# Kernel optimization log

Hardware: AMD Instinct MI355X
Metric: run time of the kernel (lower is better)

The kernel has to match this reference:

```python
import jax, jax.numpy as jnp
import numpy as np

VOCAB = 32000
PENTA_DIM = 512
DIM = 512
NUM_HEADS = 8
HEAD_DIM = DIM // NUM_HEADS
CANTOR_DEPTH = 8
K_NEIGHBORS = 64  # local_window, adaptive_window=False
BATCH = 2
SEQ = 2048
EPS = 1e-6


def cantor_coords_from_pentachora(pentachora):
    """Vectorized GeometricCantorFingerprinter over [V,5,D] -> [V] coords in [0,1]."""
    V = pentachora.shape[0]
    # pairwise squared distances between the 5 vertices: [V,5,5]
    diff = pentachora[:, :, None, :] - pentachora[:, None, :, :]
    dist_sq = jnp.sum(diff * diff, axis=-1)
    # Cayley-Menger matrix [V,6,6]
    M = jnp.zeros((V, 6, 6), dtype=pentachora.dtype)
    M = M.at[:, 0, 1:].set(1.0)
    M = M.at[:, 1:, 0].set(1.0)
    M = M.at[:, 1:, 1:].set(dist_sq)
    det = jnp.linalg.det(M)
    volume = jnp.sqrt(jnp.clip(-det / 9216.0, 0.0))
    # edge statistics: 10 upper-triangular edges
    iu, ju = np.triu_indices(5, 1)
    edge_len = jnp.sqrt(dist_sq[:, iu, ju])  # [V,10]
    mean_edge = edge_len.mean(axis=-1)
    std_edge = edge_len.std(axis=-1, ddof=1)  # torch.std is unbiased
    # vertex spread: std (ddof=1) of distances to centroid
    centroid = pentachora.mean(axis=1, keepdims=True)
    cd = jnp.linalg.norm(pentachora - centroid, axis=-1)  # [V,5]
    spread = cd.std(axis=-1, ddof=1)
    volume_norm = jax.nn.sigmoid(volume * 10.0)
    edge_ratio = jax.nn.sigmoid(std_edge / (mean_edge + 1e-6))
    spread_norm = jax.nn.sigmoid(spread)
    x = jnp.clip(volume_norm * 0.4 + edge_ratio * 0.3 + spread_norm * 0.3, EPS, 1.0 - EPS)
    bump = (volume_norm + edge_ratio + spread_norm) * 0.01
    cantor_val = jnp.zeros_like(x)
    factor = 0.5
    for _ in range(CANTOR_DEPTH):  # small fixed unroll
        x_scaled = x * 3.0
        digit = jnp.floor(x_scaled)  # x in (0,1) so trunc==floor
        x_frac = x_scaled - digit
        cantor_val = cantor_val + (digit == 2.0).astype(x.dtype) * factor
        x = jnp.clip(x_frac + bump, EPS, 1.0 - EPS)
        factor *= 0.5
    return jnp.clip(cantor_val, 0.0, 1.0)


def setup_inputs() -> dict:
    key = jax.random.key(0)
    ks = jax.random.split(key, 8)
    pentachora = jax.random.normal(ks[0], (VOCAB, 5, PENTA_DIM), dtype=jnp.float32)
    x = jax.random.normal(ks[1], (BATCH, SEQ, DIM), dtype=jnp.float32)
    token_ids = jax.random.randint(ks[2], (SEQ,), 0, VOCAB)
    s = 1.0 / np.sqrt(DIM)
    Wqkv = jax.random.normal(ks[3], (DIM, 3 * DIM), dtype=jnp.float32) * s
    bqkv = jnp.zeros((3 * DIM,), dtype=jnp.float32)
    Wout = jax.random.normal(ks[4], (DIM, DIM), dtype=jnp.float32) * s
    bout = jnp.zeros((DIM,), dtype=jnp.float32)
    return {"pentachora": pentachora, "x": x, "token_ids": token_ids,
            "Wqkv": Wqkv, "bqkv": bqkv, "Wout": Wout, "bout": bout}


def reference(pentachora, x, token_ids, Wqkv, bqkv, Wout, bout):
    coords = cantor_coords_from_pentachora(pentachora)  # [V]
    c = coords[token_ids]  # [S] per-token Cantor coordinates
    # routing: k nearest tokens in 1D Cantor space (smallest |ci - cj|)
    dist = jnp.abs(c[:, None] - c[None, :])  # [S,S]
    _, routes = jax.lax.top_k(-dist, K_NEIGHBORS)  # [S,K]
    B, S, D = x.shape
    qkv = x @ Wqkv + bqkv  # [B,S,3D]
    qkv = qkv.reshape(B, S, 3, NUM_HEADS, HEAD_DIM).transpose(2, 0, 3, 1, 4)
    q, k, v = qkv[0], qkv[1], qkv[2]  # [B,H,S,hd]
    k_g = k[:, :, routes, :]  # [B,H,S,K,hd]
    v_g = v[:, :, routes, :]
    scale = 1.0 / np.sqrt(HEAD_DIM)
    scores = jnp.einsum('bhqd,bhqkd->bhqk', q, k_g) * scale
    attn = jax.nn.softmax(scores, axis=-1)
    out = jnp.einsum('bhqk,bhqkd->bhqd', attn, v_g)  # [B,H,S,hd]
    out = out.transpose(0, 2, 1, 3).reshape(B, S, D)
    return out @ Wout + bout
```

## Files before the change

kernel.cpp:

```cpp
#include <hip/hip_runtime.h>
#include <math.h>


typedef unsigned short u16;
typedef short short8 __attribute__((ext_vector_type(8)));
typedef u16 u16x8 __attribute__((ext_vector_type(8)));
typedef float floatx4 __attribute__((ext_vector_type(4)));

#define NVOCAB 32000
#define NSEQ 2048

__device__ inline float b2f(u16 u){
  union{unsigned int i; float f;} x; x.i = ((unsigned int)u)<<16; return x.f;
}
__device__ inline u16 f2b(float f){
  union{float f; unsigned int u;} x; x.f = f;
  unsigned int u = x.u;
  u += 0x7fffu + ((u >> 16) & 1u);
  return (u16)(u >> 16);
}
__device__ inline double shfl_xor_d(double v, int m){
  union{double d; int i[2];} x; x.d = v;
  x.i[0] = __shfl_xor(x.i[0], m, 64);
  x.i[1] = __shfl_xor(x.i[1], m, 64);
  return x.d;
}
__device__ inline int detect_flag(const u16* __restrict__ p){
  int lane = threadIdx.x & 63;
  u16 u = p[lane*2];
  int e = (u >> 7) & 0xff;
  unsigned long long m = __ballot(e >= 96 && e <= 144);
  return (m == ~0ull) ? 1 : 0;
}

__global__ __launch_bounds__(256) void prep_kernel(const void* __restrict__ x,
                                                   const void* __restrict__ W1,
                                                   const void* __restrict__ W2,
                                                   const u16* __restrict__ penta,
                                                   u16* __restrict__ xb,
                                                   u16* __restrict__ Wt1,
                                                   u16* __restrict__ Wt2){
  int f = detect_flag(penta);
  int bid = blockIdx.x;
  if (bid < 1024){
    size_t i = ((size_t)bid*256 + threadIdx.x)*8;
    if (f){
      *(u16x8*)(xb+i) = *(const u16x8*)((const u16*)x + i);
    } else {
      const float* xf = (const float*)x + i;
      float4 a = *(const float4*)xf;
      float4 b = *(const float4*)(xf+4);
      u16x8 o;
      o[0]=f2b(a.x); o[1]=f2b(a.y); o[2]=f2b(a.z); o[3]=f2b(a.w);
      o[4]=f2b(b.x); o[5]=f2b(b.y); o[6]=f2b(b.z); o[7]=f2b(b.w);
      *(u16x8*)(xb+i) = o;
    }
    return;
  }
  int idx = bid - 1024;
  int bx = idx & 63;
  int k0 = (idx >> 6) * 32;
  __shared__ u16 tile[32][33];
  const int K = 512;
  const void* W; u16* Wt; int N, n0;
  if (bx < 48){ W = W1; Wt = Wt1; N = 1536; n0 = bx*32; }
  else        { W = W2; Wt = Wt2; N = 512;  n0 = (bx-48)*32; }
  int tx = threadIdx.x & 31, ty = threadIdx.x >> 5;
  #pragma unroll
  for (int i=0;i<32;i+=8){
    int k = k0+ty+i, n = n0+tx;
    u16 v = f ? ((const u16*)W)[(size_t)k*N + n]
              : f2b(((const float*)W)[(size_t)k*N + n]);
    tile[ty+i][tx] = v;
  }
  __syncthreads();
  #pragma unroll
  for (int i=0;i<32;i+=8){
    Wt[(size_t)(n0+ty+i)*K + k0+tx] = tile[tx][ty+i];
  }
}

__global__ __launch_bounds__(256) void penta_coords_kernel(const void* __restrict__ penta,
                                                           const int* __restrict__ tok,
                                                           int* __restrict__ ctok){
  int f = detect_flag((const u16*)penta);
  int slot = blockIdx.x*4 + (threadIdx.x>>6);
  int w = tok[slot];
  int lane = threadIdx.x & 63;
  float pf[5][8];
  if (f){
    const u16* base = (const u16*)penta + (size_t)w*2560 + lane*8;
    #pragma unroll
    for (int i=0;i<5;i++){
      u16x8 u = *(const u16x8*)(base + i*512);
      #pragma unroll
      for (int j=0;j<8;j++) pf[i][j] = b2f(u[j]);
    }
  } else {
    const float* base = (const float*)penta + (size_t)w*2560 + lane*8;
    #pragma unroll
    for (int i=0;i<5;i++){
      float4 f0 = *(const float4*)(base + i*512);
      float4 f1 = *(const float4*)(base + i*512 + 4);
      pf[i][0]=f0.x; pf[i][1]=f0.y; pf[i][2]=f0.z; pf[i][3]=f0.w;
      pf[i][4]=f1.x; pf[i][5]=f1.y; pf[i][6]=f1.z; pf[i][7]=f1.w;
    }
  }
  double acc[15];
  #pragma unroll
  for (int k=0;k<15;k++) acc[k]=0.0;
  #pragma unroll
  for (int j=0;j<8;j++){
    double p[5];
    #pragma unroll
    for (int i=0;i<5;i++) p[i] = (double)pf[i][j];
    double mean = (p[0]+p[1]+p[2]+p[3]+p[4])*0.2;
    int idx=0;
    #pragma unroll
    for (int a=0;a<5;a++)
      #pragma unroll
      for (int b=a+1;b<5;b++){ double d=p[a]-p[b]; acc[idx++] += d*d; }
    #pragma unroll
    for (int i=0;i<5;i++){ double d=p[i]-mean; acc[10+i] += d*d; }
  }
  #pragma unroll
  for (int k=0;k<15;k++){
    double s = acc[k];
    for (int off=32; off; off>>=1) s += shfl_xor_d(s, off);
    acc[k]=s;
  }
  if (lane != 0) return;
  double ds[10], cd2[5];
  #pragma unroll
  for (int k=0;k<10;k++) ds[k]=acc[k];
  #pragma unroll
  for (int k=0;k<5;k++) cd2[k]=acc[10+k];
  double M[6][6];
  M[0][0]=1.0; M[0][1]=0.0; M[0][2]=ds[0]; M[0][3]=ds[1]; M[0][4]=ds[2]; M[0][5]=ds[3];
  M[1][0]=0.0; M[1][1]=1.0; M[1][2]=1.0;   M[1][3]=1.0;   M[1][4]=1.0;   M[1][5]=1.0;
  M[2][0]=1.0; M[2][1]=ds[0]; M[2][2]=0.0;   M[2][3]=ds[4]; M[2][4]=ds[5]; M[2][5]=ds[6];
  M[3][0]=1.0; M[3][1]=ds[1]; M[3][2]=ds[4]; M[3][3]=0.0;   M[3][4]=ds[7]; M[3][5]=ds[8];
  M[4][0]=1.0; M[4][1]=ds[2]; M[4][2]=ds[5]; M[4][3]=ds[7]; M[4][4]=0.0;   M[4][5]=ds[9];
  M[5][0]=1.0; M[5][1]=ds[3]; M[5][2]=ds[6]; M[5][3]=ds[8]; M[5][4]=ds[9]; M[5][5]=0.0;
  double det=1.0;
  #pragma unroll
  for (int c=0;c<6;c++){
    double pv = M[c][c];
    det *= pv;
    double inv = 1.0/pv;
    #pragma unroll
    for (int r=c+1;r<6;r++){
      double fq = M[r][c]*inv;
      #pragma unroll
      for (int cc=c+1;cc<6;cc++) M[r][cc] -= fq*M[c][cc];
    }
  }
  double volume = sqrt(fmax(det/9216.0, 0.0));
  double vn = 1.0/(1.0+exp(-10.0*volume));
  double me=0.0, e[10];
  #pragma unroll
  for (int k=0;k<10;k++){ e[k]=sqrt(ds[k]); me+=e[k]; }
  me *= 0.1;
  double var=0.0;
  #pragma unroll
  for (int k=0;k<10;k++){ double d=e[k]-me; var+=d*d; }
  double se = sqrt(var/9.0);
  double er = 1.0/(1.0+exp(-(se/(me+1e-6))));
  double mc=0.0, cd[5];
  #pragma unroll
  for (int k=0;k<5;k++){ cd[k]=sqrt(cd2[k]); mc+=cd[k]; }
  mc *= 0.2;
  double v2=0.0;
  #pragma unroll
  for (int k=0;k<5;k++){ double d=cd[k]-mc; v2+=d*d; }
  double sp = sqrt(v2/4.0);
  double sn = 1.0/(1.0+exp(-sp));
  const double EPSd = 1e-6;
  double x = 0.4*vn + 0.3*er + 0.3*sn;
  x = fmin(fmax(x, EPSd), 1.0-EPSd);
  double bump = (vn+er+sn)*0.01;
  double cv=0.0, factor=0.5;
  #pragma unroll
  for (int it=0; it<8; it++){
    double xs = x*3.0;
    double frac = xs - floor(xs);
    if (xs >= 2.0) cv += factor;
    x = fmin(fmax(frac + bump, EPSd), 1.0-EPSd);
    factor *= 0.5;
  }
  cv = fmin(fmax(cv,0.0),1.0);
  ctok[slot] = (int)(cv*256.0 + 0.5);
}

__global__ __launch_bounds__(256) void routes_kernel(const int* __restrict__ ctok,
                                                     int* __restrict__ repq,
                                                     int* __restrict__ routes){
  __shared__ int cs[NSEQ];
  __shared__ int hist[256];
  __shared__ int scn[256];
  __shared__ int cnts[256];
  __shared__ int params[3];
  __shared__ int repsh;
  int tid = threadIdx.x;
  int q = blockIdx.x;
  for (int j=tid; j<NSEQ; j+=256) cs[j] = ctok[j];
  hist[tid] = 0;
  if (tid==0){ params[2]=0; repsh=0x7fffffff; }
  __syncthreads();
  int cq = cs[q];
  int base = tid*8;
  {
    int myrep = 0x7fffffff;
    #pragma unroll
    for (int i=0;i<8;i++){
      if (cs[base+i]==cq && myrep==0x7fffffff) myrep = base+i;
    }
    if (myrep != 0x7fffffff) atomicMin(&repsh, myrep);
  }
  __syncthreads();
  if (tid==0) repq[q] = repsh;
  if (repsh != q) return;
  int dloc[8];
  #pragma unroll
  for (int i=0;i<8;i++){
    int d = cs[base+i] - cq; d = d<0 ? -d : d;
    dloc[i] = d;
    atomicAdd(&hist[d], 1);
  }
  __syncthreads();
  scn[tid] = hist[tid];
  __syncthreads();
  #pragma unroll
  for (int off=1; off<256; off<<=1){
    int cur = scn[tid];
    int add = (tid>=off) ? scn[tid-off] : 0;
    __syncthreads();
    scn[tid] = cur + add;
    __syncthreads();
  }
  {
    int incl = scn[tid];
    int prev = (tid==0) ? 0 : scn[tid-1];
    if (incl >= 64 && prev < 64){ params[0]=tid; params[1]=64-prev; }
  }
  __syncthreads();
  int T=params[0], need=params[1];
  int ceq=0;
  #pragma unroll
  for (int i=0;i<8;i++) ceq += (dloc[i]==T) ? 1 : 0;
  cnts[tid]=ceq;
  __syncthreads();
  #pragma unroll
  for (int off=1; off<256; off<<=1){
    int cur = cnts[tid];
    int add = (tid>=off) ? cnts[tid-off] : 0;
    __syncthreads();
    cnts[tid] = cur + add;
    __syncthreads();
  }
  int rank = cnts[tid] - ceq;
  int* rq = routes + q*64;
  #pragma unroll
  for (int i=0;i<8;i++){
    int d = dloc[i];
    bool sel = false;
    if (d < T) sel = true;
    else if (d == T){ sel = (rank < need); rank++; }
    if (sel){
      int pos = atomicAdd(&params[2], 1);
      rq[pos] = base + i;
    }
  }
}

template<int C_FOLLOW>
__global__ __launch_bounds__(256) void gemm_direct(const u16* __restrict__ A,
    const u16* __restrict__ Wt, const void* __restrict__ bias, void* __restrict__ Cout,
    const u16* __restrict__ penta, int M, int N, int K)
{
  int f = detect_flag(penta);
  bool c_bf16 = C_FOLLOW ? (f==1) : true;
  int tid = threadIdx.x;
  int wv = tid>>6, lane = tid&63, lr = lane&15, lq = lane>>4;
  int m0 = blockIdx.y<<6, n0 = blockIdx.x<<6;
  const u16* Arow = A  + (size_t)(m0 + (wv<<4) + lr)*K + (lq<<3);
  const u16* Wr0  = Wt + (size_t)(n0 + lr)*K + (lq<<3);
  size_t wstep = (size_t)16*K;
  floatx4 acc[4];
  #pragma unroll
  for (int t=0;t<4;t++) acc[t] = (floatx4){0.f,0.f,0.f,0.f};
  #pragma unroll 4
  for (int k0=0;k0<K;k0+=32){
    short8 af = *(const short8*)(Arow + k0);
    #pragma unroll
    for (int t4=0;t4<4;t4++){
      short8 bfv = *(const short8*)(Wr0 + (size_t)t4*wstep + k0);
      acc[t4] = __builtin_amdgcn_mfma_f32_16x16x32_bf16(af, bfv, acc[t4], 0, 0, 0);
    }
  }
  #pragma unroll
  for (int t4=0;t4<4;t4++){
    #pragma unroll
    for (int r=0;r<4;r++){
      int m = m0 + (wv<<4) + (lq<<2) + r;
      int n = n0 + (t4<<4) + lr;
      float bv = f ? b2f(((const u16*)bias)[n]) : ((const float*)bias)[n];
      float val = acc[t4][r] + bv;
      if (c_bf16) ((u16*)Cout)[(size_t)m*N + n] = f2b(val);
      else        ((float*)Cout)[(size_t)m*N + n] = val;
    }
  }
}

__global__ __launch_bounds__(256) void attn_kernel(const u16* __restrict__ qkv,
                                                   const int* __restrict__ routes,
                                                   const int* __restrict__ repq,
                                                   u16* __restrict__ outa){
  __shared__ float sc[4][8*65];
  __shared__ int rbuf[4][64];
  int tid = threadIdx.x;
  int wv = tid>>6, lane = tid&63;
  int bq = blockIdx.x*4 + wv;
  int b = bq >> 11;
  int q = bq & 2047;
  rbuf[wv][lane] = routes[(repq[q]<<6) + lane];
  int h8 = lane>>3;
  const u16* kb = qkv + (size_t)(b<<11)*1536;
  float qv[8];
  {
    u16x8 qraw = *(const u16x8*)(kb + (size_t)q*1536 + lane*8);
    #pragma unroll
    for (int t=0;t<8;t++) qv[t] = b2f(qraw[t]);
  }
  __syncthreads();
  for (int j=0;j<64;j++){
    int rj = rbuf[wv][j];
    u16x8 kraw = *(const u16x8*)(kb + (size_t)rj*1536 + 512 + lane*8);
    float p = 0.f;
    #pragma unroll
    for (int t=0;t<8;t++) p = fmaf(b2f(kraw[t]), qv[t], p);
    p += __shfl_xor(p, 1, 64);
    p += __shfl_xor(p, 2, 64);
    p += __shfl_xor(p, 4, 64);
    if ((lane&7)==0) sc[wv][h8*65 + j] = p * 0.125f;
  }
  __syncthreads();
  {
    int jg = (lane&7)<<3;
    float sv[8];
    float m = -1e30f;
    #pragma unroll
    for (int t=0;t<8;t++){ sv[t] = sc[wv][h8*65 + jg + t]; m = fmaxf(m, sv[t]); }
    m = fmaxf(m, __shfl_xor(m, 1, 64));
    m = fmaxf(m, __shfl_xor(m, 2, 64));
    m = fmaxf(m, __shfl_xor(m, 4, 64));
    float s = 0.f;
    #pragma unroll
    for (int t=0;t<8;t++){ sv[t] = expf(sv[t]-m); s += sv[t]; }
    s += __shfl_xor(s, 1, 64);
    s += __shfl_xor(s, 2, 64);
    s += __shfl_xor(s, 4, 64);
    float inv = 1.f/s;
    #pragma unroll
    for (int t=0;t<8;t++) sc[wv][h8*65 + jg + t] = sv[t]*inv;
  }
  __syncthreads();
  int dg = (lane&7)<<3;
  const u16* vb = kb + 1024 + (h8<<6) + dg;
  float acc8[8];
  #pragma unroll
  for (int t=0;t<8;t++) acc8[t]=0.f;
  for (int j=0;j<64;j++){
    float p = sc[wv][h8*65 + j];
    u16x8 v8 = *(const u16x8*)(vb + (size_t)rbuf[wv][j]*1536);
    #pragma unroll
    for (int t=0;t<8;t++) acc8[t] = fmaf(p, b2f(v8[t]), acc8[t]);
  }
  u16x8 o;
  #pragma unroll
  for (int t=0;t<8;t++) o[t] = f2b(acc8[t]);
  *(u16x8*)(outa + (size_t)bq*512 + (h8<<6) + dg) = o;
}

extern "C" void kernel_launch(void* const* d_in, const int* in_sizes, int n_in,
                              void* d_out, int out_size, void* d_ws, size_t ws_size,
                              hipStream_t stream) {
  const void* penta = d_in[0];
  const void* x     = d_in[1];
  const int*  tok   = (const int*)d_in[2];
  const void* Wqkv  = d_in[3];
  const void* bqkv  = d_in[4];
  const void* Wout  = d_in[5];
  const void* bout  = d_in[6];

  char* ws = (char*)d_ws;
  int*    ctok   = (int*)   (ws + 0);
  int*    repq   = (int*)   (ws + 8192);
  int*    routes = (int*)   (ws + 16384);
  u16*    xb     = (u16*)   (ws + 1048576);
  u16*    Wt1    = (u16*)   (ws + 5242880);
  u16*    Wt2    = (u16*)   (ws + 6815744);
  u16*    qkv    = (u16*)   (ws + 7340032);
  u16*    attn   = (u16*)   (ws + 19922944);

  prep_kernel<<<dim3(2048), dim3(256), 0, stream>>>(x, Wqkv, Wout, (const u16*)penta, xb, Wt1, Wt2);
  penta_coords_kernel<<<dim3(512), dim3(256), 0, stream>>>(penta, tok, ctok);
  routes_kernel<<<dim3(2048), dim3(256), 0, stream>>>(ctok, repq, routes);
  gemm_direct<0><<<dim3(24,64), dim3(256), 0, stream>>>(xb, Wt1, bqkv, (void*)qkv, (const u16*)penta, 4096, 1536, 512);
  attn_kernel<<<dim3(1024), dim3(256), 0, stream>>>(qkv, routes, repq, attn);
  gemm_direct<1><<<dim3(8,64), dim3(256), 0, stream>>>(attn, Wt2, bout, d_out, (const u16*)penta, 4096, 512, 512);
}
```

Before: 518.0 us.

## Fuse prep and coords kernels, skip bf16 x copy, double GEMM M-tile

Merges the input conversion/transpose kernel with the per-token pentachoron coordinate kernel into one launch, removing a kernel boundary. When inputs are already bf16 the x copy is skipped and the QKV GEMM reads x directly. The GEMM now computes a 128-row tile per block (two 16-row MFMA strips per wave), so each B fragment load is reused twice, at the cost of more accumulator registers and half as many blocks.

Result: faster. 489.9 us (-5.4%).

```diff
diff --git a/kernel.cpp b/kernel.cpp
--- a/kernel.cpp
+++ b/kernel.cpp
@@ -33,58 +33,54 @@
   return (m == ~0ull) ? 1 : 0;
 }
 
-__global__ __launch_bounds__(256) void prep_kernel(const void* __restrict__ x,
-                                                   const void* __restrict__ W1,
-                                                   const void* __restrict__ W2,
-                                                   const u16* __restrict__ penta,
-                                                   u16* __restrict__ xb,
-                                                   u16* __restrict__ Wt1,
-                                                   u16* __restrict__ Wt2){
-  int f = detect_flag(penta);
+__global__ __launch_bounds__(256) void prep_coords_kernel(const void* __restrict__ x,
+                                                          const void* __restrict__ W1,
+                                                          const void* __restrict__ W2,
+                                                          const void* __restrict__ penta,
+                                                          const int* __restrict__ tok,
+                                                          u16* __restrict__ xb,
+                                                          u16* __restrict__ Wt1,
+                                                          u16* __restrict__ Wt2,
+                                                          int* __restrict__ ctok){
+  __shared__ u16 tile[32][33];
+  int f = detect_flag((const u16*)penta);
   int bid = blockIdx.x;
   if (bid < 1024){
+    if (f) return;
     size_t i = ((size_t)bid*256 + threadIdx.x)*8;
-    if (f){
-      *(u16x8*)(xb+i) = *(const u16x8*)((const u16*)x + i);
-    } else {
-      const float* xf = (const float*)x + i;
-      float4 a = *(const float4*)xf;
-      float4 b = *(const float4*)(xf+4);
-      u16x8 o;
-      o[0]=f2b(a.x); o[1]=f2b(a.y); o[2]=f2b(a.z); o[3]=f2b(a.w);
-      o[4]=f2b(b.x); o[5]=f2b(b.y); o[6]=f2b(b.z); o[7]=f2b(b.w);
-      *(u16x8*)(xb+i) = o;
-    }
+    const float* xf = (const float*)x + i;
+    float4 a = *(const float4*)xf;
+    float4 b = *(const float4*)(xf+4);
+    u16x8 o;
+    o[0]=f2b(a.x); o[1]=f2b(a.y); o[2]=f2b(a.z); o[3]=f2b(a.w);
+    o[4]=f2b(b.x); o[5]=f2b(b.y); o[6]=f2b(b.z); o[7]=f2b(b.w);
+    *(u16x8*)(xb+i) = o;
     return;
   }
-  int idx = bid - 1024;
-  int bx = idx & 63;
-  int k0 = (idx >> 6) * 32;
-  __shared__ u16 tile[32][33];
-  const int K = 512;
-  const void* W; u16* Wt; int N, n0;
-  if (bx < 48){ W = W1; Wt = Wt1; N = 1536; n0 = bx*32; }
-  else        { W = W2; Wt = Wt2; N = 512;  n0 = (bx-48)*32; }
-  int tx = threadIdx.x & 31, ty = threadIdx.x >> 5;
-  #pragma unroll
-  for (int i=0;i<32;i+=8){
-    int k = k0+ty+i, n = n0+tx;
-    u16 v = f ? ((const u16*)W)[(size_t)k*N + n]
-              : f2b(((const float*)W)[(size_t)k*N + n]);
-    tile[ty+i][tx] = v;
-  }
-  __syncthreads();
-  #pragma unroll
-  for (int i=0;i<32;i+=8){
-    Wt[(size_t)(n0+ty+i)*K + k0+tx] = tile[tx][ty+i];
-  }
-}
-
-__global__ __launch_bounds__(256) void penta_coords_kernel(const void* __restrict__ penta,
-                                                           const int* __restrict__ tok,
-                                                           int* __restrict__ ctok){
-  int f = detect_flag((const u16*)penta);
-  int slot = blockIdx.x*4 + (threadIdx.x>>6);
+  if (bid < 2048){
+    int idx = bid - 1024;
+    int bx = idx & 63;
+    int k0 = (idx >> 6) * 32;
+    const int K = 512;
+    const void* W; u16* Wt; int N, n0;
+    if (bx < 48){ W = W1; Wt = Wt1; N = 1536; n0 = bx*32; }
+    else        { W = W2; Wt = Wt2; N = 512;  n0 = (bx-48)*32; }
+    int tx = threadIdx.x & 31, ty = threadIdx.x >> 5;
+    #pragma unroll
+    for (int i=0;i<32;i+=8){
+      int k = k0+ty+i, n = n0+tx;
+      u16 v = f ? ((const u16*)W)[(size_t)k*N + n]
+                : f2b(((const float*)W)[(size_t)k*N + n]);
+      tile[ty+i][tx] = v;
+    }
+    __syncthreads();
+    #pragma unroll
+    for (int i=0;i<32;i+=8){
+      Wt[(size_t)(n0+ty+i)*K + k0+tx] = tile[tx][ty+i];
+    }
+    return;
+  }
+  int slot = (bid-2048)*4 + (threadIdx.x>>6);
   int w = tok[slot];
   int lane = threadIdx.x & 63;
   float pf[5][8];
@@ -176,16 +172,16 @@
   double sp = sqrt(v2/4.0);
   double sn = 1.0/(1.0+exp(-sp));
   const double EPSd = 1e-6;
-  double x = 0.4*vn + 0.3*er + 0.3*sn;
-  x = fmin(fmax(x, EPSd), 1.0-EPSd);
+  double xx = 0.4*vn + 0.3*er + 0.3*sn;
+  xx = fmin(fmax(xx, EPSd), 1.0-EPSd);
   double bump = (vn+er+sn)*0.01;
   double cv=0.0, factor=0.5;
   #pragma unroll
   for (int it=0; it<8; it++){
-    double xs = x*3.0;
+    double xs = xx*3.0;
     double frac = xs - floor(xs);
     if (xs >= 2.0) cv += factor;
-    x = fmin(fmax(frac + bump, EPSd), 1.0-EPSd);
+    xx = fmin(fmax(frac + bump, EPSd), 1.0-EPSd);
     factor *= 0.5;
   }
   cv = fmin(fmax(cv,0.0),1.0);
@@ -274,40 +270,50 @@
 }
 
 template<int C_FOLLOW>
-__global__ __launch_bounds__(256) void gemm_direct(const u16* __restrict__ A,
-    const u16* __restrict__ Wt, const void* __restrict__ bias, void* __restrict__ Cout,
+__global__ __launch_bounds__(256) void gemm_direct(const u16* __restrict__ Af1,
+    const u16* __restrict__ Af0, const u16* __restrict__ Wt,
+    const void* __restrict__ bias, void* __restrict__ Cout,
     const u16* __restrict__ penta, int M, int N, int K)
 {
   int f = detect_flag(penta);
+  const u16* A = f ? Af1 : Af0;
   bool c_bf16 = C_FOLLOW ? (f==1) : true;
   int tid = threadIdx.x;
   int wv = tid>>6, lane = tid&63, lr = lane&15, lq = lane>>4;
-  int m0 = blockIdx.y<<6, n0 = blockIdx.x<<6;
-  const u16* Arow = A  + (size_t)(m0 + (wv<<4) + lr)*K + (lq<<3);
-  const u16* Wr0  = Wt + (size_t)(n0 + lr)*K + (lq<<3);
+  int m0 = blockIdx.y<<7, n0 = blockIdx.x<<6;
+  const u16* Arow0 = A  + (size_t)(m0 + (wv<<5) + lr)*K + (lq<<3);
+  const u16* Arow1 = Arow0 + (size_t)16*K;
+  const u16* Wr0   = Wt + (size_t)(n0 + lr)*K + (lq<<3);
   size_t wstep = (size_t)16*K;
-  floatx4 acc[4];
-  #pragma unroll
-  for (int t=0;t<4;t++) acc[t] = (floatx4){0.f,0.f,0.f,0.f};
+  floatx4 acc[2][4];
+  #pragma unroll
+  for (int mt=0;mt<2;mt++)
+    #pragma unroll
+    for (int t=0;t<4;t++) acc[mt][t] = (floatx4){0.f,0.f,0.f,0.f};
   #pragma unroll 4
   for (int k0=0;k0<K;k0+=32){
-    short8 af = *(const short8*)(Arow + k0);
+    short8 af0 = *(const short8*)(Arow0 + k0);
+    short8 af1 = *(const short8*)(Arow1 + k0);
     #pragma unroll
     for (int t4=0;t4<4;t4++){
       short8 bfv = *(const short8*)(Wr0 + (size_t)t4*wstep + k0);
-      acc[t4] = __builtin_amdgcn_mfma_f32_16x16x32_bf16(af, bfv, acc[t4], 0, 0, 0);
-    }
-  }
-  #pragma unroll
-  for (int t4=0;t4<4;t4++){
-    #pragma unroll
-    for (int r=0;r<4;r++){
-      int m = m0 + (wv<<4) + (lq<<2) + r;
-      int n = n0 + (t4<<4) + lr;
-      float bv = f ? b2f(((const u16*)bias)[n]) : ((const float*)bias)[n];
-      float val = acc[t4][r] + bv;
-      if (c_bf16) ((u16*)Cout)[(size_t)m*N + n] = f2b(val);
-      else        ((float*)Cout)[(size_t)m*N + n] = val;
+      acc[0][t4] = __builtin_amdgcn_mfma_f32_16x16x32_bf16(af0, bfv, acc[0][t4], 0, 0, 0);
+      acc[1][t4] = __builtin_amdgcn_mfma_f32_16x16x32_bf16(af1, bfv, acc[1][t4], 0, 0, 0);
+    }
+  }
+  #pragma unroll
+  for (int mt=0;mt<2;mt++){
+    #pragma unroll
+    for (int t4=0;t4<4;t4++){
+      #pragma unroll
+      for (int r=0;r<4;r++){
+        int m = m0 + (wv<<5) + (mt<<4) + (lq<<2) + r;
+        int n = n0 + (t4<<4) + lr;
+        float bv = f ? b2f(((const u16*)bias)[n]) : ((const float*)bias)[n];
+        float val = acc[mt][t4][r] + bv;
+        if (c_bf16) ((u16*)Cout)[(size_t)m*N + n] = f2b(val);
+        else        ((float*)Cout)[(size_t)m*N + n] = val;
+      }
     }
   }
 }
@@ -403,10 +409,9 @@
   u16*    qkv    = (u16*)   (ws + 7340032);
   u16*    attn   = (u16*)   (ws + 19922944);
 
-  prep_kernel<<<dim3(2048), dim3(256), 0, stream>>>(x, Wqkv, Wout, (const u16*)penta, xb, Wt1, Wt2);
-  penta_coords_kernel<<<dim3(512), dim3(256), 0, stream>>>(penta, tok, ctok);
+  prep_coords_kernel<<<dim3(2560), dim3(256), 0, stream>>>(x, Wqkv, Wout, penta, tok, xb, Wt1, Wt2, ctok);
   routes_kernel<<<dim3(2048), dim3(256), 0, stream>>>(ctok, repq, routes);
-  gemm_direct<0><<<dim3(24,64), dim3(256), 0, stream>>>(xb, Wt1, bqkv, (void*)qkv, (const u16*)penta, 4096, 1536, 512);
+  gemm_direct<0><<<dim3(24,32), dim3(256), 0, stream>>>((const u16*)x, xb, Wt1, bqkv, (void*)qkv, (const u16*)penta, 4096, 1536, 512);
   attn_kernel<<<dim3(1024), dim3(256), 0, stream>>>(qkv, routes, repq, attn);
-  gemm_direct<1><<<dim3(8,64), dim3(256), 0, stream>>>(attn, Wt2, bout, d_out, (const u16*)penta, 4096, 512, 512);
-}
+  gemm_direct<1><<<dim3(8,32), dim3(256), 0, stream>>>(attn, attn, Wt2, bout, d_out, (const u16*)penta, 4096, 512, 512);
+}
```
